# Optimization experiments

Hardware: AMD Instinct MI355X
Metric: run time of the kernel (lower is better)

## Reference

```python
import jax, jax.numpy as jnp
import numpy as np

GRAPH_BIAS_SCALE = 0.8
CTX_GATE_STRENGTH = 2.0
COMMITMENT_COST = 0.25
DECAY = 0.99

N = 262144      # flattened batch*seq tokens
LAT = 128       # latent_dim
DIM = 2 * LAT   # concat(real, imag)
K_SYN = 64
K_SEM = 128


def setup_inputs() -> dict:
    key = jax.random.key(0)
    ks = jax.random.split(key, 18)
    f = jnp.float32
    return {
        "z_fast_re": jax.random.normal(ks[0], (N, LAT), f),
        "z_fast_im": jax.random.normal(ks[1], (N, LAT), f),
        "z_slow_re": jax.random.normal(ks[2], (N, LAT), f),
        "z_slow_im": jax.random.normal(ks[3], (N, LAT), f),
        "cb_syn": jax.random.normal(ks[4], (K_SYN, DIM), f),
        "cb_sem": jax.random.normal(ks[5], (K_SEM, DIM), f),
        "W_syn": jax.random.normal(ks[6], (DIM, K_SYN), f) / np.sqrt(DIM),
        "b_syn": jnp.zeros((K_SYN,), f),
        "W_sem": jax.random.normal(ks[7], (DIM, K_SEM), f) / np.sqrt(DIM),
        "b_sem": jnp.zeros((K_SEM,), f),
        "cl_syn": jnp.zeros((K_SYN,), f),
        "avg_syn": jax.random.normal(ks[8], (K_SYN, DIM), f),
        "cl_sem": jnp.zeros((K_SEM,), f),
        "avg_sem": jax.random.normal(ks[9], (K_SEM, DIM), f),
        "adj_syn": jnp.zeros((K_SYN, K_SYN), f),
        "adj_sem": jnp.zeros((K_SEM, K_SEM), f),
        "prev_syn": jax.random.randint(ks[10], (N,), 0, K_SYN, jnp.int32),
        "prev_sem": jax.random.randint(ks[11], (N,), 0, K_SEM, jnp.int32),
    }


def _vq_step(z_re, z_im, cb, W, b, cl, avg, adj, prev):
    """One context-gated VQ step (training mode). Returns straight-through
    quantized flat latent, loss, indices, and the updated buffers/codebook."""
    K = cb.shape[0]
    zf = jnp.concatenate([z_re, z_im], axis=-1)          # [N, DIM]
    # squared-distance matrix [N, K]
    d = (jnp.sum(zf * zf, axis=1, keepdims=True)
         + jnp.sum(cb * cb, axis=1)
         - 2.0 * zf @ cb.T)
    bias_history = jax.nn.sigmoid(adj[prev])             # [N, K] gather
    bias_context = jax.nn.softmax(zf @ W + b, axis=-1)   # [N, K]
    d = d - (GRAPH_BIAS_SCALE * bias_history + CTX_GATE_STRENGTH * bias_context)
    idx = jnp.argmin(d, axis=1)                          # [N]
    z_q = cb[idx]                                        # [N, DIM] gather
    adj_new = adj.at[prev, idx].set(adj[prev, idx] * 0.995 + 1.0)
    # EMA codebook update (uses detached stats; mutates after z_q already gathered)
    counts = jnp.zeros((K,), zf.dtype).at[idx].add(1.0)          # enc.sum(0)
    embed_sum = jnp.zeros((K, zf.shape[1]), zf.dtype).at[idx].add(zf)  # enc.T @ zf
    cl_new = cl * DECAY + (1.0 - DECAY) * counts
    avg_new = avg * DECAY + (1.0 - DECAY) * embed_sum
    n = jnp.sum(cl_new)
    cs = (cl_new + 1e-6) / (n + K * 1e-6) * n
    cb_new = avg_new / cs[:, None]
    # losses use z_q from the OLD codebook (gathered before the EMA copy)
    sg = jax.lax.stop_gradient
    loss = (jnp.mean((sg(z_q) - zf) ** 2)
            + COMMITMENT_COST * jnp.mean((z_q - sg(zf)) ** 2))
    zq_st = zf + sg(z_q - zf)                            # straight-through
    return zq_st, loss, idx, cl_new, avg_new, cb_new, adj_new


def reference(z_fast_re, z_fast_im, z_slow_re, z_slow_im,
              cb_syn, cb_sem, W_syn, b_syn, W_sem, b_sem,
              cl_syn, avg_syn, cl_sem, avg_sem, adj_syn, adj_sem,
              prev_syn, prev_sem):
    zq_syn, loss_syn, idx_syn, cl_syn_n, avg_syn_n, cb_syn_n, adj_syn_n = _vq_step(
        z_fast_re, z_fast_im, cb_syn, W_syn, b_syn, cl_syn, avg_syn, adj_syn, prev_syn)
    zq_sem, loss_sem, idx_sem, cl_sem_n, avg_sem_n, cb_sem_n, adj_sem_n = _vq_step(
        z_slow_re, z_slow_im, cb_sem, W_sem, b_sem, cl_sem, avg_sem, adj_sem, prev_sem)
    # zq_* are the flat (real||imag) representation of the complex outputs
    return (zq_syn, zq_sem, loss_syn + loss_sem, idx_syn, idx_sem,
            cb_syn_n, cl_syn_n, avg_syn_n, adj_syn_n,
            cb_sem_n, cl_sem_n, avg_sem_n, adj_sem_n)
```

## Files before the change

kernel.cpp:

```cpp
#include <hip/hip_runtime.h>

#define N_TOK 262144
#define LATD  128
#define DIMD  256

using f32x4  = __attribute__((ext_vector_type(4)))  float;
using f32x16 = __attribute__((ext_vector_type(16))) float;
using f16x8  = __attribute__((ext_vector_type(8)))  _Float16;
using f16x2  = __attribute__((ext_vector_type(2)))  _Float16;

#define W_PACK_SYN 0
#define W_PACK_SEM 32768
#define W_CBN_SYN  98304
#define W_CBN_SEM  98368
#define W_IDX_SYN  98496
#define W_IDX_SEM  360640
#define W_CNT_SYN  622784
#define W_CNT_SEM  622848
#define W_EMB_SYN  622976
#define W_EMB_SEM  639360
#define W_MRK_SYN  672128
#define W_MRK_SEM  676224
#define W_LOSSP_SYN 692612
#define W_LOSSP_SEM 700804
#define W_ZERO_BEG 622784
#define W_ZERO_END 692612

#define OFF_ZQ_SYN  0LL
#define OFF_ZQ_SEM  67108864LL
#define OFF_LOSS    134217728LL
#define OFF_IDX_SYN 134217729LL
#define OFF_IDX_SEM 134479873LL
#define OFF_CB_SYN  134742017LL
#define OFF_CL_SYN  134758401LL
#define OFF_AVG_SYN 134758465LL
#define OFF_ADJ_SYN 134774849LL
#define OFF_CB_SEM  134778945LL
#define OFF_CL_SEM  134811713LL
#define OFF_AVG_SEM 134811841LL
#define OFF_ADJ_SEM 134844609LL

template <int K>
__device__ void prep_pack_body(int bid2, const float* __restrict__ cb,
                               const float* __restrict__ W, _Float16* __restrict__ pack) {
  constexpr int NCT = 2 * K / 32;
  constexpr int PER_KT = NCT * 512;
  int t = bid2 * 256 + threadIdx.x;
  int kt = t / PER_KT;
  int r  = t - kt * PER_KT;
  int l  = (r >> 3) & 63;
  int e  = r & 7;
  int ct = r >> 9;
  int j   = kt * 16 + (l >> 5) * 8 + e;
  int col = ct * 32 + (l & 31);
  float x = (col < K) ? cb[col * DIMD + j] : W[j * K + (col - K)];
  _Float16 h = (_Float16)x;
  _Float16 lo = (_Float16)(x - (float)h);
  pack[(size_t)kt * 2 * PER_KT + r]          = h;
  pack[(size_t)kt * 2 * PER_KT + PER_KT + r] = lo;
}

__global__ __launch_bounds__(256) void k_prep(
    const float* __restrict__ cbs, const float* __restrict__ cbm,
    const float* __restrict__ Wsy, const float* __restrict__ Wse,
    float* __restrict__ ws, _Float16* __restrict__ packs, _Float16* __restrict__ packm) {
  __shared__ float red[256];
  const int bid = blockIdx.x, tid = threadIdx.x;
  if (bid < 273) {
    int idx = W_ZERO_BEG + bid * 256 + tid;
    if (idx < W_ZERO_END) ws[idx] = 0.0f;
  } else if (bid < 401) {
    prep_pack_body<64>(bid - 273, cbs, Wsy, packs);
  } else if (bid < 657) {
    prep_pack_body<128>(bid - 401, cbm, Wse, packm);
  } else {
    int k = bid - 657;
    const float* src; float* dst;
    if (k < 64) { src = cbs + (size_t)k * DIMD; dst = ws + W_CBN_SYN + k; }
    else        { src = cbm + (size_t)(k - 64) * DIMD; dst = ws + W_CBN_SEM + (k - 64); }
    float v = src[tid];
    red[tid] = v * v;
    __syncthreads();
    for (int s = 128; s > 0; s >>= 1) {
      if (tid < s) red[tid] += red[tid + s];
      __syncthreads();
    }
    if (tid == 0) *dst = red[0];
  }
}

template <int K>
__device__ void passA_body(int bid,
    const float* __restrict__ zre, const float* __restrict__ zim,
    const _Float16* __restrict__ pack, const float* __restrict__ cbn,
    const float* __restrict__ cb,  const float* __restrict__ bvec,
    const float* __restrict__ adj, const int* __restrict__ prev,
    float* __restrict__ zq_out, float* __restrict__ idxf_out,
    int* __restrict__ idxi_ws, int* __restrict__ mark_ws,
    float* __restrict__ lossp, float* wred) {
  constexpr int NCT = K / 16;
  constexpr int NH  = K / 32;
  constexpr int PER_KT = NCT * 512;
  const int tid  = threadIdx.x;
  const int lane = tid & 63;
  const int wv   = tid >> 6;
  const int kg   = lane >> 5;
  const int j    = lane & 31;
  const int t0   = bid * 128 + wv * 32;
  const int gt   = t0 + j;

  f32x16 acc[NCT];
#pragma unroll
  for (int t = 0; t < NCT; ++t)
#pragma unroll
    for (int r = 0; r < 16; ++r) acc[t][r] = 0.0f;
  float zn = 0.0f;

  f32x4 v0, v1, nv0, nv1;
  {
    const float* zp = zre + (size_t)gt * LATD + kg * 8;
    v0 = *(const f32x4*)zp;
    v1 = *(const f32x4*)(zp + 4);
  }
#pragma unroll 2
  for (int kt = 0; kt < 16; ++kt) {
    if (kt + 1 < 16) {
      const float* zsrc2 = (kt + 1 < 8) ? zre : zim;
      const float* zp2 = zsrc2 + (size_t)gt * LATD + ((kt + 1) & 7) * 16 + kg * 8;
      nv0 = *(const f32x4*)zp2;
      nv1 = *(const f32x4*)(zp2 + 4);
    }
    f16x8 Bh, Bl;
#pragma unroll
    for (int e = 0; e < 4; ++e) {
      _Float16 h0 = (_Float16)v0[e];
      Bh[e] = h0;       Bl[e] = (_Float16)(v0[e] - (float)h0);
      _Float16 h1 = (_Float16)v1[e];
      Bh[e + 4] = h1;   Bl[e + 4] = (_Float16)(v1[e] - (float)h1);
      zn += v0[e] * v0[e];
      zn += v1[e] * v1[e];
    }
    const _Float16* pk = pack + (size_t)kt * 2 * PER_KT + lane * 8;
#pragma unroll
    for (int t = 0; t < NCT; ++t) {
      f16x8 Ah = *(const f16x8*)(pk + (size_t)t * 512);
      f16x8 Al = *(const f16x8*)(pk + PER_KT + (size_t)t * 512);
      acc[t] = __builtin_amdgcn_mfma_f32_32x32x16_f16(Ah, Bh, acc[t], 0, 0, 0);
      acc[t] = __builtin_amdgcn_mfma_f32_32x32x16_f16(Ah, Bl, acc[t], 0, 0, 0);
      acc[t] = __builtin_amdgcn_mfma_f32_32x32x16_f16(Al, Bh, acc[t], 0, 0, 0);
    }
    v0 = nv0; v1 = nv1;
  }

  const int pv = prev[gt];

  float mx = -1e30f;
#pragma unroll
  for (int t = 0; t < NH; ++t)
#pragma unroll
    for (int q = 0; q < 4; ++q) {
      f32x4 bv4 = *(const f32x4*)&bvec[t * 32 + 8 * q + 4 * kg];
#pragma unroll
      for (int b = 0; b < 4; ++b) {
        acc[NH + t][4 * q + b] += bv4[b];
        mx = fmaxf(mx, acc[NH + t][4 * q + b]);
      }
    }
  mx = fmaxf(mx, __shfl_xor(mx, 32));
  float es = 0.0f;
#pragma unroll
  for (int t = 0; t < NH; ++t)
#pragma unroll
    for (int r = 0; r < 16; ++r) {
      acc[NH + t][r] = __expf(acc[NH + t][r] - mx);
      es += acc[NH + t][r];
    }
  es += __shfl_xor(es, 32);
  const float inv = 1.0f / es;

  const float* adjrow = adj + (size_t)pv * K;
  float best = -1e30f; int bidx = 0; float bdot = 0.0f;
#pragma unroll
  for (int t = 0; t < NH; ++t)
#pragma unroll
    for (int q = 0; q < 4; ++q) {
      const int e0 = t * 32 + 8 * q + 4 * kg;
      f32x4 cb4v = *(const f32x4*)&cbn[e0];
      f32x4 ad4  = *(const f32x4*)&adjrow[e0];
#pragma unroll
      for (int b = 0; b < 4; ++b) {
        int r = 4 * q + b;
        float dot = acc[t][r];
        float sg  = 1.0f / (1.0f + __expf(-ad4[b]));
        float sc  = dot - 0.5f * cb4v[b] + 0.4f * sg + acc[NH + t][r] * inv;
        int   e   = e0 + b;
        if (sc > best || (sc == best && e < bidx)) {
          best = sc; bidx = e; bdot = dot;
        }
      }
    }
  {
    float ob = __shfl_xor(best, 32);
    int   oi = __shfl_xor(bidx, 32);
    float od = __shfl_xor(bdot, 32);
    if (ob > best || (ob == best && oi < bidx)) { best = ob; bidx = oi; bdot = od; }
  }
  const float znf = zn + __shfl_xor(zn, 32);

  float lj = 0.0f;
  if (lane < 32) {
    idxf_out[gt] = (float)bidx;
    idxi_ws[gt]  = bidx;
    mark_ws[pv * K + bidx] = 1;
    lj = cbn[bidx] + znf - 2.0f * bdot;
  }
#pragma unroll
  for (int off = 32; off; off >>= 1) lj += __shfl_xor(lj, off);
  if (lane == 0) wred[wv] = lj;

  const float4* cb4p = (const float4*)cb;
  float4* zq4 = (float4*)zq_out;
#pragma unroll 4
  for (int i = 0; i < 32; ++i) {
    int bi_i = __shfl(bidx, i);
    zq4[(size_t)(t0 + i) * 64 + lane] = cb4p[(size_t)bi_i * 64 + lane];
  }
  __syncthreads();
  if (tid == 0) lossp[bid] = wred[0] + wred[1] + wred[2] + wred[3];
}

__global__ __launch_bounds__(256, 2) void k_passA_all(
    const float* __restrict__ zfre, const float* __restrict__ zfim,
    const float* __restrict__ zsre, const float* __restrict__ zsim,
    const _Float16* __restrict__ packs, const _Float16* __restrict__ packm,
    const float* __restrict__ cbns, const float* __restrict__ cbnm,
    const float* __restrict__ cbs, const float* __restrict__ cbm,
    const float* __restrict__ bsy, const float* __restrict__ bse,
    const float* __restrict__ adjs, const float* __restrict__ adjm,
    const int* __restrict__ prvs, const int* __restrict__ prvm,
    float* __restrict__ zqs, float* __restrict__ zqm,
    float* __restrict__ idxfs, float* __restrict__ idxfm,
    int* __restrict__ idxis, int* __restrict__ idxim,
    int* __restrict__ mrks, int* __restrict__ mrkm,
    float* __restrict__ lossps, float* __restrict__ losspm) {
  __shared__ float wred[4];
  const int bid = blockIdx.x >> 1;
  if ((blockIdx.x & 1) == 0)
    passA_body<64>(bid, zfre, zfim, packs, cbns, cbs, bsy, adjs, prvs,
                   zqs, idxfs, idxis, mrks, lossps, wred);
  else
    passA_body<128>(bid, zsre, zsim, packm, cbnm, cbm, bse, adjm, prvm,
                    zqm, idxfm, idxim, mrkm, losspm, wred);
}

template <int K>
__device__ void passB_body(int fid,
    const float* __restrict__ zre, const float* __restrict__ zim,
    const int* __restrict__ idxi,
    float* __restrict__ emb_ws, int* __restrict__ cnt_ws,
    int* idxl, int* cntl, unsigned short* zT) {
  constexpr int TPB  = 2048;
  constexpr int CH   = 128;
  constexpr int NCT2 = (K == 64) ? 1 : 2;
  const int tid  = threadIdx.x;
  const int lane = tid & 63, wv = tid >> 6;
  const int cg    = fid & 3;
  const int chunk = fid >> 2;
  const int tbase = chunk * TPB;

  if (tid < K) cntl[tid] = 0;
  __syncthreads();
#pragma unroll
  for (int i = 0; i < TPB / 256; ++i) {
    int id = idxi[tbase + i * 256 + tid];
    idxl[i * 256 + tid] = id;
    if (cg == 0) atomicAdd(&cntl[id], 1);
  }
  __syncthreads();
  if (cg == 0 && tid < K) atomicAdd(&cnt_ws[tid], cntl[tid]);

  const int rt  = (K == 64) ? (wv & 1) : wv;
  const int ct0 = (K == 64) ? (wv >> 1) : 0;
  const int krow = rt * 32 + (lane & 31);
  const int kg   = lane >> 5;
  const float* zsrc = (cg < 2) ? zre : zim;
  const int cbase = (cg & 1) * 64;

  f32x16 acc[NCT2];
#pragma unroll
  for (int c = 0; c < NCT2; ++c)
#pragma unroll
    for (int r = 0; r < 16; ++r) acc[c][r] = 0.0f;

  const int sq = tid & 15;
  const int sp = tid >> 4;

  auto stage = [&](int sc) {
    unsigned short* zb = zT + (sc & 1) * 8192;
#pragma unroll
    for (int it = 0; it < 4; ++it) {
      int p = sp + it * 16;
      int t = sc * CH + 2 * p;
      const float* zr = zsrc + (size_t)(tbase + t) * LATD + cbase + 4 * sq;
      f32x4 a = *(const f32x4*)zr;
      f32x4 b = *(const f32x4*)(zr + LATD);
#pragma unroll
      for (int c4 = 0; c4 < 4; ++c4) {
        int c = 4 * sq + c4;
        f16x2 pr;
        pr[0] = (_Float16)a[c4];
        pr[1] = (_Float16)b[c4];
        int byte = c * 256 + ((4 * p) ^ ((c & 7) << 4));
        *(f16x2*)((char*)zb + byte) = pr;
      }
    }
  };

  stage(0);
  for (int sc = 0; sc < TPB / CH; ++sc) {
    __syncthreads();
    if (sc + 1 < TPB / CH) stage(sc + 1);
    const unsigned short* zb = zT + (sc & 1) * 8192;
#pragma unroll
    for (int st = 0; st < 8; ++st) {
      const int tloc = sc * CH + st * 16 + kg * 8;
      f16x8 Af;
#pragma unroll
      for (int e = 0; e < 8; ++e)
        Af[e] = (idxl[tloc + e] == krow) ? (_Float16)1.0f : (_Float16)0.0f;
#pragma unroll
      for (int c = 0; c < NCT2; ++c) {
        int col = (ct0 + c) * 32 + (lane & 31);
        int byte = col * 256 + ((st * 32 + kg * 16) ^ ((col & 7) << 4));
        f16x8 Bf = *(const f16x8*)((const char*)zb + byte);
        acc[c] = __builtin_amdgcn_mfma_f32_32x32x16_f16(Af, Bf, acc[c], 0, 0, 0);
      }
    }
  }
#pragma unroll
  for (int c = 0; c < NCT2; ++c)
#pragma unroll
    for (int r = 0; r < 16; ++r) {
      int row = rt * 32 + (r & 3) + 8 * (r >> 2) + 4 * (lane >> 5);
      int col = cg * 64 + (ct0 + c) * 32 + (lane & 31);
      atomicAdd(&emb_ws[row * DIMD + col], acc[c][r]);
    }
}

__global__ __launch_bounds__(256) void k_passB_all(
    const float* __restrict__ zfre, const float* __restrict__ zfim,
    const float* __restrict__ zsre, const float* __restrict__ zsim,
    const int* __restrict__ idxis, const int* __restrict__ idxim,
    float* __restrict__ embs, float* __restrict__ embm,
    int* __restrict__ cnts, int* __restrict__ cntm) {
  __shared__ int idxl[2048];
  __shared__ int cntl[128];
  __shared__ __align__(16) unsigned short zT[2 * 8192];
  const int fid = blockIdx.x >> 1;
  if ((blockIdx.x & 1) == 0)
    passB_body<64>(fid, zfre, zfim, idxis, embs, cnts, idxl, cntl, zT);
  else
    passB_body<128>(fid, zsre, zsim, idxim, embm, cntm, idxl, cntl, zT);
}

__global__ __launch_bounds__(256) void k_fin(
    const float* __restrict__ ws, const float* __restrict__ clsi, const float* __restrict__ clmi,
    const float* __restrict__ avgs, const float* __restrict__ avgm,
    const float* __restrict__ adjs, const float* __restrict__ adjm,
    float* __restrict__ o_loss, float* __restrict__ o_cl_syn, float* __restrict__ o_cl_sem,
    float* __restrict__ o_cb_syn, float* __restrict__ o_avg_syn, float* __restrict__ o_adj_syn,
    float* __restrict__ o_cb_sem, float* __restrict__ o_avg_sem, float* __restrict__ o_adj_sem) {
  __shared__ float sred[256];
  const int* wsi = (const int*)ws;
  const int bid = blockIdx.x, tid = threadIdx.x;
  if (bid == 0) {
    float s = 0.0f;
    for (int i = tid; i < 2048; i += 256) s += ws[W_LOSSP_SYN + i];
    for (int i = tid; i < 2048; i += 256) s += ws[W_LOSSP_SEM + i];
    sred[tid] = s;
    __syncthreads();
    for (int st = 128; st > 0; st >>= 1) {
      if (tid < st) sred[tid] += sred[tid + st];
      __syncthreads();
    }
    if (tid < 64)
      o_cl_syn[tid] = clsi[tid] * 0.99f + 0.01f * (float)wsi[W_CNT_SYN + tid];
    if (tid < 128)
      o_cl_sem[tid] = clmi[tid] * 0.99f + 0.01f * (float)wsi[W_CNT_SEM + tid];
    if (tid == 0)
      *o_loss = 1.25f * sred[0] / ((float)N_TOK * 256.0f);
    return;
  }
  const int e = (bid - 1) * 256 + tid;
  float n = 0.0f;
  if (e < 49152) {
    const bool syn = e < 16384;
    const int KK = syn ? 64 : 128;
    const float* clp = syn ? clsi : clmi;
    const int cntoff = syn ? W_CNT_SYN : W_CNT_SEM;
    float v = 0.0f;
    if (tid < KK) v = clp[tid] * 0.99f + 0.01f * (float)wsi[cntoff + tid];
    sred[tid] = v;
    __syncthreads();
    for (int st = 128; st > 0; st >>= 1) {
      if (tid < st) sred[tid] += sred[tid + st];
      __syncthreads();
    }
    n = sred[0];
  }
  if (e < 16384) {
    int k = e >> 8;
    float av = avgs[e] * 0.99f + 0.01f * ws[W_EMB_SYN + e];
    o_avg_syn[e] = av;
    float cnt = (float)wsi[W_CNT_SYN + k];
    float cl  = clsi[k] * 0.99f + 0.01f * cnt;
    float cs  = (cl + 1e-6f) / (n + (float)(64 * 1e-6)) * n;
    o_cb_syn[e] = av / cs;
  } else if (e < 49152) {
    int e2 = e - 16384;
    int k = e2 >> 8;
    float av = avgm[e2] * 0.99f + 0.01f * ws[W_EMB_SEM + e2];
    o_avg_sem[e2] = av;
    float cnt = (float)wsi[W_CNT_SEM + k];
    float cl  = clmi[k] * 0.99f + 0.01f * cnt;
    float cs  = (cl + 1e-6f) / (n + (float)(128 * 1e-6)) * n;
    o_cb_sem[e2] = av / cs;
  } else if (e < 53248) {
    int a = e - 49152;
    float old = adjs[a];
    o_adj_syn[a] = wsi[W_MRK_SYN + a] ? old * 0.995f + 1.0f : old;
  } else if (e < 69632) {
    int a = e - 53248;
    float old = adjm[a];
    o_adj_sem[a] = wsi[W_MRK_SEM + a] ? old * 0.995f + 1.0f : old;
  }
}

extern "C" void kernel_launch(void* const* d_in, const int* in_sizes, int n_in,
                              void* d_out, int out_size, void* d_ws, size_t ws_size,
                              hipStream_t stream) {
  const float* zfre = (const float*)d_in[0];
  const float* zfim = (const float*)d_in[1];
  const float* zsre = (const float*)d_in[2];
  const float* zsim = (const float*)d_in[3];
  const float* cbs  = (const float*)d_in[4];
  const float* cbm  = (const float*)d_in[5];
  const float* Wsy  = (const float*)d_in[6];
  const float* bsy  = (const float*)d_in[7];
  const float* Wse  = (const float*)d_in[8];
  const float* bse  = (const float*)d_in[9];
  const float* clsi = (const float*)d_in[10];
  const float* avgs = (const float*)d_in[11];
  const float* clmi = (const float*)d_in[12];
  const float* avgm = (const float*)d_in[13];
  const float* adjs = (const float*)d_in[14];
  const float* adjm = (const float*)d_in[15];
  const int*   prvs = (const int*)d_in[16];
  const int*   prvm = (const int*)d_in[17];

  float* out = (float*)d_out;
  float* wsf = (float*)d_ws;
  int*   wsi = (int*)d_ws;
  _Float16* wsh = (_Float16*)d_ws;

  k_prep<<<849, 256, 0, stream>>>(cbs, cbm, Wsy, Wse, wsf,
      wsh + 2 * W_PACK_SYN, wsh + 2 * W_PACK_SEM);

  k_passA_all<<<4096, 256, 0, stream>>>(
      zfre, zfim, zsre, zsim,
      wsh + 2 * W_PACK_SYN, wsh + 2 * W_PACK_SEM,
      wsf + W_CBN_SYN, wsf + W_CBN_SEM,
      cbs, cbm, bsy, bse, adjs, adjm, prvs, prvm,
      out + OFF_ZQ_SYN, out + OFF_ZQ_SEM,
      out + OFF_IDX_SYN, out + OFF_IDX_SEM,
      wsi + W_IDX_SYN, wsi + W_IDX_SEM,
      wsi + W_MRK_SYN, wsi + W_MRK_SEM,
      wsf + W_LOSSP_SYN, wsf + W_LOSSP_SEM);

  k_passB_all<<<1024, 256, 0, stream>>>(
      zfre, zfim, zsre, zsim,
      wsi + W_IDX_SYN, wsi + W_IDX_SEM,
      wsf + W_EMB_SYN, wsf + W_EMB_SEM,
      wsi + W_CNT_SYN, wsi + W_CNT_SEM);

  k_fin<<<273, 256, 0, stream>>>(wsf, clsi, clmi, avgs, avgm, adjs, adjm,
      out + OFF_LOSS, out + OFF_CL_SYN, out + OFF_CL_SEM,
      out + OFF_CB_SYN, out + OFF_AVG_SYN, out + OFF_ADJ_SYN,
      out + OFF_CB_SEM, out + OFF_AVG_SEM, out + OFF_ADJ_SEM);
}
```

Measured before the change: 613.2 us.

## Stage packed codebook tiles in LDS via async global_load_lds double buffering

Pass A now copies each k-tile of the packed fp16 hi/lo codebook+W matrix into shared memory with global_load_lds, double-buffered, and reads MFMA A operands from LDS instead of global memory per wave. The fused syn/sem kernel is also split into two templated launches so each has its own LDS size. The aim is to cut redundant global/L2 traffic across the four waves. In exchange it adds a block barrier per k iteration and larger LDS use, which may lower occupancy. It also serialises the two codebook passes across launches.

```diff
diff --git a/kernel.cpp b/kernel.cpp
--- a/kernel.cpp
+++ b/kernel.cpp
@@ -39,6 +39,12 @@
 #define OFF_CL_SEM  134811713LL
 #define OFF_AVG_SEM 134811841LL
 #define OFF_ADJ_SEM 134844609LL
+
+__device__ inline void gload16(const void* g, void* l) {
+  __builtin_amdgcn_global_load_lds(
+      (const __attribute__((address_space(1))) unsigned int*)g,
+      (__attribute__((address_space(3))) unsigned int*)l, 16, 0, 0);
+}
 
 template <int K>
 __device__ void prep_pack_body(int bid2, const float* __restrict__ cb,
@@ -90,24 +96,38 @@
 }
 
 template <int K>
-__device__ void passA_body(int bid,
+__global__ __launch_bounds__(256, 2) void k_passA(
     const float* __restrict__ zre, const float* __restrict__ zim,
     const _Float16* __restrict__ pack, const float* __restrict__ cbn,
     const float* __restrict__ cb,  const float* __restrict__ bvec,
     const float* __restrict__ adj, const int* __restrict__ prev,
     float* __restrict__ zq_out, float* __restrict__ idxf_out,
     int* __restrict__ idxi_ws, int* __restrict__ mark_ws,
-    float* __restrict__ lossp, float* wred) {
+    float* __restrict__ lossp) {
   constexpr int NCT = K / 16;
   constexpr int NH  = K / 32;
   constexpr int PER_KT = NCT * 512;
+  constexpr int CHUNK = 2 * PER_KT;
+  constexpr int SITERS = CHUNK * 2 / 4096;
+  __shared__ __align__(16) _Float16 packl[2 * CHUNK];
+  __shared__ float wred[4];
+
   const int tid  = threadIdx.x;
   const int lane = tid & 63;
   const int wv   = tid >> 6;
   const int kg   = lane >> 5;
   const int j    = lane & 31;
-  const int t0   = bid * 128 + wv * 32;
+  const int t0   = blockIdx.x * 128 + wv * 32;
   const int gt   = t0 + j;
+
+  auto stage = [&](int kt) {
+    const _Float16* src = pack + (size_t)kt * CHUNK;
+    char* dst = (char*)packl + (kt & 1) * CHUNK * 2;
+#pragma unroll
+    for (int i = 0; i < SITERS; ++i)
+      gload16(src + (size_t)(i * 256 + tid) * 8,
+              dst + ((i * 256 + (tid & 192)) << 4));
+  };
 
   f32x16 acc[NCT];
 #pragma unroll
@@ -116,14 +136,16 @@
     for (int r = 0; r < 16; ++r) acc[t][r] = 0.0f;
   float zn = 0.0f;
 
+  stage(0);
   f32x4 v0, v1, nv0, nv1;
   {
     const float* zp = zre + (size_t)gt * LATD + kg * 8;
     v0 = *(const f32x4*)zp;
     v1 = *(const f32x4*)(zp + 4);
   }
-#pragma unroll 2
   for (int kt = 0; kt < 16; ++kt) {
+    __syncthreads();
+    if (kt + 1 < 16) stage(kt + 1);
     if (kt + 1 < 16) {
       const float* zsrc2 = (kt + 1 < 8) ? zre : zim;
       const float* zp2 = zsrc2 + (size_t)gt * LATD + ((kt + 1) & 7) * 16 + kg * 8;
@@ -140,11 +162,11 @@
       zn += v0[e] * v0[e];
       zn += v1[e] * v1[e];
     }
-    const _Float16* pk = pack + (size_t)kt * 2 * PER_KT + lane * 8;
+    const _Float16* Bp = packl + (kt & 1) * CHUNK;
 #pragma unroll
     for (int t = 0; t < NCT; ++t) {
-      f16x8 Ah = *(const f16x8*)(pk + (size_t)t * 512);
-      f16x8 Al = *(const f16x8*)(pk + PER_KT + (size_t)t * 512);
+      f16x8 Ah = *(const f16x8*)(Bp + (size_t)t * 512 + lane * 8);
+      f16x8 Al = *(const f16x8*)(Bp + PER_KT + (size_t)t * 512 + lane * 8);
       acc[t] = __builtin_amdgcn_mfma_f32_32x32x16_f16(Ah, Bh, acc[t], 0, 0, 0);
       acc[t] = __builtin_amdgcn_mfma_f32_32x32x16_f16(Ah, Bl, acc[t], 0, 0, 0);
       acc[t] = __builtin_amdgcn_mfma_f32_32x32x16_f16(Al, Bh, acc[t], 0, 0, 0);
@@ -226,31 +248,7 @@
     zq4[(size_t)(t0 + i) * 64 + lane] = cb4p[(size_t)bi_i * 64 + lane];
   }
   __syncthreads();
-  if (tid == 0) lossp[bid] = wred[0] + wred[1] + wred[2] + wred[3];
-}
-
-__global__ __launch_bounds__(256, 2) void k_passA_all(
-    const float* __restrict__ zfre, const float* __restrict__ zfim,
-    const float* __restrict__ zsre, const float* __restrict__ zsim,
-    const _Float16* __restrict__ packs, const _Float16* __restrict__ packm,
-    const float* __restrict__ cbns, const float* __restrict__ cbnm,
-    const float* __restrict__ cbs, const float* __restrict__ cbm,
-    const float* __restrict__ bsy, const float* __restrict__ bse,
-    const float* __restrict__ adjs, const float* __restrict__ adjm,
-    const int* __restrict__ prvs, const int* __restrict__ prvm,
-    float* __restrict__ zqs, float* __restrict__ zqm,
-    float* __restrict__ idxfs, float* __restrict__ idxfm,
-    int* __restrict__ idxis, int* __restrict__ idxim,
-    int* __restrict__ mrks, int* __restrict__ mrkm,
-    float* __restrict__ lossps, float* __restrict__ losspm) {
-  __shared__ float wred[4];
-  const int bid = blockIdx.x >> 1;
-  if ((blockIdx.x & 1) == 0)
-    passA_body<64>(bid, zfre, zfim, packs, cbns, cbs, bsy, adjs, prvs,
-                   zqs, idxfs, idxis, mrks, lossps, wred);
-  else
-    passA_body<128>(bid, zsre, zsim, packm, cbnm, cbm, bse, adjm, prvm,
-                    zqm, idxfm, idxim, mrkm, losspm, wred);
+  if (tid == 0) lossp[blockIdx.x] = wred[0] + wred[1] + wred[2] + wred[3];
 }
 
 template <int K>
@@ -466,16 +464,14 @@
   k_prep<<<849, 256, 0, stream>>>(cbs, cbm, Wsy, Wse, wsf,
       wsh + 2 * W_PACK_SYN, wsh + 2 * W_PACK_SEM);
 
-  k_passA_all<<<4096, 256, 0, stream>>>(
-      zfre, zfim, zsre, zsim,
-      wsh + 2 * W_PACK_SYN, wsh + 2 * W_PACK_SEM,
-      wsf + W_CBN_SYN, wsf + W_CBN_SEM,
-      cbs, cbm, bsy, bse, adjs, adjm, prvs, prvm,
-      out + OFF_ZQ_SYN, out + OFF_ZQ_SEM,
-      out + OFF_IDX_SYN, out + OFF_IDX_SEM,
-      wsi + W_IDX_SYN, wsi + W_IDX_SEM,
-      wsi + W_MRK_SYN, wsi + W_MRK_SEM,
-      wsf + W_LOSSP_SYN, wsf + W_LOSSP_SEM);
+  k_passA<64><<<N_TOK / 128, 256, 0, stream>>>(
+      zfre, zfim, wsh + 2 * W_PACK_SYN, wsf + W_CBN_SYN, cbs, bsy, adjs, prvs,
+      out + OFF_ZQ_SYN, out + OFF_IDX_SYN, wsi + W_IDX_SYN, wsi + W_MRK_SYN,
+      wsf + W_LOSSP_SYN);
+  k_passA<128><<<N_TOK / 128, 256, 0, stream>>>(
+      zsre, zsim, wsh + 2 * W_PACK_SEM, wsf + W_CBN_SEM, cbm, bse, adjm, prvm,
+      out + OFF_ZQ_SEM, out + OFF_IDX_SEM, wsi + W_IDX_SEM, wsi + W_MRK_SEM,
+      wsf + W_LOSSP_SEM);
 
   k_passB_all<<<1024, 256, 0, stream>>>(
       zfre, zfim, zsre, zsim,
```

Result: faster. 505.7 us, median of 3 (-17.5%).
